# Kernel optimization log

Hardware: AMD Instinct MI355X
Metric: run time of the kernel (lower is better)

The kernel has to match this reference:

```python
import jax, jax.numpy as jnp
import numpy as np

B = 512        # graphs per batch
N_NODES = 64   # nodes per graph
IN_CH = 256
EMBED = 64
TOPK = 20
NEG_SLOPE = 0.2


def setup_inputs() -> dict:
    key = jax.random.key(0)
    ks = jax.random.split(key, 6)
    N = B * N_NODES
    x = jax.random.normal(ks[0], (N, IN_CH), dtype=jnp.float32)
    # fully-connected graph WITH self loops, per graph, sorted source-major
    src = jnp.repeat(jnp.arange(N_NODES, dtype=jnp.int32), N_NODES)  # [n*n]
    dst = jnp.tile(jnp.arange(N_NODES, dtype=jnp.int32), N_NODES)    # [n*n]
    offs = (jnp.arange(B, dtype=jnp.int32) * N_NODES)[:, None]       # [B,1]
    l = (src[None, :] + offs).reshape(-1)
    r = (dst[None, :] + offs).reshape(-1)
    edge_index = jnp.stack([l, r]).astype(jnp.int32)                 # [2, B*n*n]
    batch = jnp.repeat(jnp.arange(B, dtype=jnp.int32), N_NODES)      # [N]
    glorot = lambda k, sh: jax.random.uniform(k, sh, jnp.float32,
                                              -1.0, 1.0) * np.sqrt(6.0 / (sh[0] + sh[-1]))
    Wl = glorot(ks[1], (EMBED, IN_CH))
    bl = jnp.zeros((EMBED,), jnp.float32)
    Wr = glorot(ks[2], (EMBED, IN_CH))
    br = jnp.zeros((EMBED,), jnp.float32)
    att = glorot(ks[3], (1, EMBED))
    return {"x": x, "edge_index": edge_index, "batch": batch,
            "Wl": Wl, "bl": bl, "Wr": Wr, "br": br, "att": att}


def reference(x, edge_index, batch, Wl, bl, Wr, br, att):
    N = x.shape[0]
    x_l = x @ Wl.T + bl                      # [N, D]
    x_r = x @ Wr.T + br                      # [N, D]
    l, r = edge_index[0], edge_index[1]
    # edge gather + GAT-style score
    e = jax.nn.leaky_relu(x_l[l] + x_r[r], negative_slope=NEG_SLOPE)  # [E, D]
    alpha = (e * att[0]).sum(axis=-1)                                  # [E]
    # segment softmax grouped by source node l (each group is non-empty)
    m = jax.ops.segment_max(alpha, l, num_segments=N)
    a = jnp.exp(alpha - m[l])
    s = jax.ops.segment_sum(a, l, num_segments=N)
    a = a / s[l]
    # kNN sparsify: zero the diagonal then per-row topk
    a3 = a.reshape(B, N_NODES, N_NODES)
    a3 = a3 * (1.0 - jnp.eye(N_NODES, dtype=a3.dtype))
    attention, indices = jax.lax.top_k(a3, TOPK)     # [B, n, k] sorted desc
    attention = attention.reshape(-1)                 # [B*n*k]
    offs = (jnp.arange(B, dtype=jnp.int32) * N_NODES)[:, None]
    index_i = (jnp.repeat(jnp.arange(N_NODES, dtype=jnp.int32), TOPK)[None, :]
               + offs).reshape(-1)
    index_j = (indices.astype(jnp.int32)
               + (jnp.arange(B, dtype=jnp.int32) * N_NODES)[:, None, None]).reshape(-1)
    new_edge_index = jnp.stack([index_i, index_j])    # [2, B*n*k]
    return new_edge_index, attention
```

## Files before the change

### kernel.cpp

```cpp
#include <hip/hip_runtime.h>
#include <stdint.h>

#define NGRAPH 512
#define NN 64
#define INCH 256
#define TOPK 20
#define EPR 655360
#define WS_NEED ((size_t)65536 + (size_t)16777216)

typedef __attribute__((ext_vector_type(8))) short bf16x8;
typedef __attribute__((ext_vector_type(4))) float f32x4;

#define XLR 0
#define XRR 4352
#define SMEM_DW 8704

static __device__ __forceinline__ uint32_t f2bfbits(float f) {
  uint32_t u = __float_as_uint(f);
  return (u + 0x7FFFu + ((u >> 16) & 1u)) >> 16;
}
static __device__ __forceinline__ uint32_t pk2(float a, float b) {
  return f2bfbits(a) | (f2bfbits(b) << 16);
}
static __device__ __forceinline__ float keyalpha(uint32_t k) {
  uint32_t ub = (k & 0x80000000u) ? (k ^ 0x80000000u) : ~k;
  return __uint_as_float(ub & 0xFFFFFFC0u);
}
static __device__ __forceinline__ float redsum64(float v) {
  int p;
  p = __builtin_amdgcn_update_dpp(0, __float_as_int(v), 0xB1, 0xF, 0xF, true);
  v += __int_as_float(p);
  p = __builtin_amdgcn_update_dpp(0, __float_as_int(v), 0x4E, 0xF, 0xF, true);
  v += __int_as_float(p);
  v += __shfl_xor(v, 4);
  v += __shfl_xor(v, 8);
  v += __shfl_xor(v, 16);
  v += __shfl_xor(v, 32);
  return v;
}

__global__ __launch_bounds__(256) void wpack2(const float* __restrict__ Wl,
                                              const float* __restrict__ Wr,
                                              uint4* __restrict__ wsW) {
  const int t = blockIdx.x * 256 + threadIdx.x;
  const int lo = t & 15, quad = (t >> 4) & 3, ct = (t >> 6) & 3;
  const int ks = (t >> 8) & 7, half = (t >> 11) & 1;
  const int n = ct * 16 + lo, k0 = ks * 32 + quad * 8;
  const float* src = half ? Wr : Wl;
  const float4* s4 = (const float4*)(src + (size_t)n * INCH + k0);
  float4 a0 = s4[0], a1 = s4[1];
  wsW[t] = (uint4){ pk2(a0.x, a0.y), pk2(a0.z, a0.w), pk2(a1.x, a1.y), pk2(a1.z, a1.w) };
}

__global__ __launch_bounds__(256) void xpack(const float* __restrict__ x,
                                             uint4* __restrict__ xp) {
  const int t = blockIdx.x * 256 + threadIdx.x;
  const int lo = t & 15, quad = (t >> 4) & 3, rt = (t >> 6) & 3;
  const int ks = (t >> 8) & 7, b = t >> 11;
  const int row = b * 64 + rt * 16 + lo, k0 = ks * 32 + quad * 8;
  const float4* s4 = (const float4*)(x + (size_t)row * INCH + k0);
  float4 a0 = s4[0], a1 = s4[1];
  xp[t] = (uint4){ pk2(a0.x, a0.y), pk2(a0.z, a0.w), pk2(a1.x, a1.y), pk2(a1.z, a1.w) };
}

template <bool XP>
__global__ __launch_bounds__(512, 4) void gat_fused(
    const float* __restrict__ x,
    const uint4* __restrict__ wsV,
    const float* __restrict__ blv,
    const float* __restrict__ brv,
    const float* __restrict__ att,
    float* __restrict__ out)
{
  __shared__ __align__(16) uint32_t smemU[SMEM_DW];
  float* smemF = (float*)smemU;

  const int b    = blockIdx.x;
  const int t    = threadIdx.x;
  const int w    = t >> 6;
  const int lane = t & 63;
  const int quad = lane >> 4;
  const int lo   = lane & 15;
  const int nodeBase = b * NN;

  const float attv = att[lane];

  const int half = w >> 2;
  const int rt   = w & 3;
  const int r0   = rt * 16;
  const uint4* xpV = wsV + 4096;

  f32x4 acc[4];
  #pragma unroll
  for (int ct = 0; ct < 4; ++ct) acc[ct] = (f32x4){0.f, 0.f, 0.f, 0.f};

  #pragma unroll
  for (int ks = 0; ks < 8; ++ks) {
    bf16x8 afrag;
    if constexpr (XP) {
      uint4 au = xpV[(size_t)b * 2048 + ks * 256 + rt * 64 + quad * 16 + lo];
      afrag = __builtin_bit_cast(bf16x8, au);
    } else {
      const int k0 = ks * 32 + quad * 8;
      const float* ap = x + (size_t)(nodeBase + r0 + lo) * INCH + k0;
      float4 a0 = *(const float4*)ap;
      float4 a1 = *(const float4*)(ap + 4);
      uint4 au = { pk2(a0.x, a0.y), pk2(a0.z, a0.w), pk2(a1.x, a1.y), pk2(a1.z, a1.w) };
      afrag = __builtin_bit_cast(bf16x8, au);
    }
    #pragma unroll
    for (int ct = 0; ct < 4; ++ct) {
      uint4 bu = wsV[half * 2048 + ks * 256 + ct * 64 + quad * 16 + lo];
      bf16x8 bfrag = __builtin_bit_cast(bf16x8, bu);
      acc[ct] = __builtin_amdgcn_mfma_f32_16x16x32_bf16(afrag, bfrag, acc[ct], 0, 0, 0);
    }
  }

  {
    const float* bias = half ? brv : blv;
    const int dstBase = half ? XRR : XLR;
    #pragma unroll
    for (int ct = 0; ct < 4; ++ct) {
      const int d = ct * 16 + lo;
      const float bb = bias[d];
      #pragma unroll
      for (int rg = 0; rg < 4; ++rg)
        smemF[dstBase + (r0 + quad * 4 + rg) * 68 + d] = acc[ct][rg] + bb;
    }
  }
  __syncthreads();

  const int rB = w * 8;

  float xlv[8];
  #pragma unroll
  for (int q = 0; q < 8; ++q)
    xlv[q] = smemF[XLR + (rB + q) * 68 + lane];

  float sl[8];
  #pragma unroll
  for (int q = 0; q < 8; ++q)
    sl[q] = redsum64(attv * xlv[q]);

  float pacc[8];
  #pragma unroll
  for (int q = 0; q < 8; ++q) pacc[q] = 0.f;
  float srp = 0.f;
  const int xrb = XRR + lane * 68;
  #pragma unroll
  for (int c = 0; c < 4; ++c) {
    f32x4 xrc[4];
    #pragma unroll
    for (int g = 0; g < 4; ++g)
      xrc[g] = *(const f32x4*)&smemF[xrb + c * 16 + g * 4];
    #pragma unroll
    for (int dl = 0; dl < 16; ++dl) {
      const int d = c * 16 + dl;
      const float xv = xrc[dl >> 2][dl & 3];
      const float av = __int_as_float(
          __builtin_amdgcn_readlane(__float_as_int(attv), d));
      srp = fmaf(av, xv, srp);
      #pragma unroll
      for (int q = 0; q < 8; ++q) {
        const float xls = __int_as_float(
            __builtin_amdgcn_readlane(__float_as_int(xlv[q]), d));
        pacc[q] = fmaf(av, fabsf(xls + xv), pacc[q]);
      }
    }
  }

  float aq[8];
  #pragma unroll
  for (int q = 0; q < 8; ++q)
    aq[q] = 0.6f * (sl[q] + srp) + 0.4f * pacc[q];

  uint32_t key[8];
  #pragma unroll
  for (int q = 0; q < 8; ++q) {
    const uint32_t u = __float_as_uint(aq[q]);
    uint32_t kk = u ^ ((uint32_t)((int32_t)u >> 31) | 0x80000000u);
    kk = (kk & 0xFFFFFFC0u) | (uint32_t)(63 - lane);
    key[q] = (lane == rB + q) ? 0u : kk;
  }

  #pragma unroll
  for (int k = 2; k <= 64; k <<= 1) {
    #pragma unroll
    for (int j = k >> 1; j >= 1; j >>= 1) {
      const bool keep_max = (((lane & k) == 0) == ((lane & j) == 0));
      #pragma unroll
      for (int q = 0; q < 8; ++q) {
        uint32_t p;
        if (j == 1)
          p = (uint32_t)__builtin_amdgcn_update_dpp(0, (int)key[q], 0xB1, 0xF, 0xF, true);
        else if (j == 2)
          p = (uint32_t)__builtin_amdgcn_update_dpp(0, (int)key[q], 0x4E, 0xF, 0xF, true);
        else
          p = (uint32_t)__shfl_xor((int)key[q], j);
        const uint32_t mx = (key[q] > p) ? key[q] : p;
        const uint32_t mn = (key[q] > p) ? p : key[q];
        key[q] = keep_max ? mx : mn;
      }
    }
  }

  float mq[8], Sq[8];
  #pragma unroll
  for (int q = 0; q < 8; ++q) {
    const uint32_t tk = (uint32_t)__builtin_amdgcn_readlane((int)key[q], 0);
    const float topa  = keyalpha(tk);
    const float adiag = __int_as_float(
        __builtin_amdgcn_readlane(__float_as_int(aq[q]), rB + q));
    mq[q] = fmaxf(topa, adiag);
    Sq[q] = redsum64(__expf(aq[q] - mq[q]));
  }

  if (lane < TOPK) {
    #pragma unroll
    for (int q = 0; q < 8; ++q) {
      const int g = nodeBase + rB + q;
      const uint32_t kq = key[q];
      const float alpha = keyalpha(kq);
      const int jj = 63 - (int)(kq & 63u);
      const float va = __expf(alpha - mq[q]) * (1.0f / Sq[q]);
      out[(size_t)g * 20 + lane] = (float)g;
      out[(size_t)EPR + (size_t)g * 20 + lane] = (float)(nodeBase + jj);
      out[2 * (size_t)EPR + (size_t)g * 20 + lane] = va;
    }
  }
}

extern "C" void kernel_launch(void* const* d_in, const int* in_sizes, int n_in,
                              void* d_out, int out_size, void* d_ws, size_t ws_size,
                              hipStream_t stream) {
  const float* x   = (const float*)d_in[0];
  const float* Wl  = (const float*)d_in[3];
  const float* bl  = (const float*)d_in[4];
  const float* Wr  = (const float*)d_in[5];
  const float* br  = (const float*)d_in[6];
  const float* att = (const float*)d_in[7];
  uint4* wsW = (uint4*)d_ws;

  wpack2<<<dim3(16), dim3(256), 0, stream>>>(Wl, Wr, wsW);
  if (ws_size >= WS_NEED) {
    xpack<<<dim3(4096), dim3(256), 0, stream>>>(x, wsW + 4096);
    gat_fused<true><<<dim3(NGRAPH), dim3(512), 0, stream>>>(
        x, wsW, bl, br, att, (float*)d_out);
  } else {
    gat_fused<false><<<dim3(NGRAPH), dim3(512), 0, stream>>>(
        x, wsW, bl, br, att, (float*)d_out);
  }
}
```

Before: 124.6 us.

## Split fused GAT kernel into GEMM and per-row alpha/top-k sort kernels

```diff
diff --git a/kernel.cpp b/kernel.cpp
--- a/kernel.cpp
+++ b/kernel.cpp
@@ -6,14 +6,11 @@
 #define INCH 256
 #define TOPK 20
 #define EPR 655360
+#define NROWS 32768
 #define WS_NEED ((size_t)65536 + (size_t)16777216)
 
 typedef __attribute__((ext_vector_type(8))) short bf16x8;
 typedef __attribute__((ext_vector_type(4))) float f32x4;
-
-#define XLR 0
-#define XRR 4352
-#define SMEM_DW 8704
 
 static __device__ __forceinline__ uint32_t f2bfbits(float f) {
   uint32_t u = __float_as_uint(f);
@@ -26,16 +23,38 @@
   uint32_t ub = (k & 0x80000000u) ? (k ^ 0x80000000u) : ~k;
   return __uint_as_float(ub & 0xFFFFFFC0u);
 }
-static __device__ __forceinline__ float redsum64(float v) {
-  int p;
-  p = __builtin_amdgcn_update_dpp(0, __float_as_int(v), 0xB1, 0xF, 0xF, true);
-  v += __int_as_float(p);
-  p = __builtin_amdgcn_update_dpp(0, __float_as_int(v), 0x4E, 0xF, 0xF, true);
-  v += __int_as_float(p);
-  v += __shfl_xor(v, 4);
-  v += __shfl_xor(v, 8);
-  v += __shfl_xor(v, 16);
-  v += __shfl_xor(v, 32);
+
+static __device__ __forceinline__ uint32_t bflyu(uint32_t v, const int j, const int lane) {
+  if (j == 1)
+    return (uint32_t)__builtin_amdgcn_update_dpp(0, (int)v, 0xB1, 0xF, 0xF, true);
+  if (j == 2)
+    return (uint32_t)__builtin_amdgcn_update_dpp(0, (int)v, 0x4E, 0xF, 0xF, true);
+  if (j == 8)
+    return (uint32_t)__builtin_amdgcn_update_dpp(0, (int)v, 0x128, 0xF, 0xF, true);
+#if __has_builtin(__builtin_amdgcn_permlane16_swap)
+  if (j == 16) {
+    auto r = __builtin_amdgcn_permlane16_swap((unsigned)v, (unsigned)v, false, false);
+    return (uint32_t)(((lane >> 4) & 1) ? r[0] : r[1]);
+  }
+#endif
+#if __has_builtin(__builtin_amdgcn_permlane32_swap)
+  if (j == 32) {
+    auto r = __builtin_amdgcn_permlane32_swap((unsigned)v, (unsigned)v, false, false);
+    return (uint32_t)((lane & 32) ? r[0] : r[1]);
+  }
+#endif
+  return (uint32_t)__shfl_xor((int)v, j);
+}
+static __device__ __forceinline__ float bflyf(float v, const int j, const int lane) {
+  return __uint_as_float(bflyu(__float_as_uint(v), j, lane));
+}
+static __device__ __forceinline__ float redsum64(float v, const int lane) {
+  v += bflyf(v, 1, lane);
+  v += bflyf(v, 2, lane);
+  v += bflyf(v, 4, lane);
+  v += bflyf(v, 8, lane);
+  v += bflyf(v, 16, lane);
+  v += bflyf(v, 32, lane);
   return v;
 }
 
@@ -52,29 +71,13 @@
   wsW[t] = (uint4){ pk2(a0.x, a0.y), pk2(a0.z, a0.w), pk2(a1.x, a1.y), pk2(a1.z, a1.w) };
 }
 
-__global__ __launch_bounds__(256) void xpack(const float* __restrict__ x,
-                                             uint4* __restrict__ xp) {
-  const int t = blockIdx.x * 256 + threadIdx.x;
-  const int lo = t & 15, quad = (t >> 4) & 3, rt = (t >> 6) & 3;
-  const int ks = (t >> 8) & 7, b = t >> 11;
-  const int row = b * 64 + rt * 16 + lo, k0 = ks * 32 + quad * 8;
-  const float4* s4 = (const float4*)(x + (size_t)row * INCH + k0);
-  float4 a0 = s4[0], a1 = s4[1];
-  xp[t] = (uint4){ pk2(a0.x, a0.y), pk2(a0.z, a0.w), pk2(a1.x, a1.y), pk2(a1.z, a1.w) };
-}
-
-template <bool XP>
-__global__ __launch_bounds__(512, 4) void gat_fused(
+__global__ __launch_bounds__(512, 4) void xlr_gemm(
     const float* __restrict__ x,
     const uint4* __restrict__ wsV,
     const float* __restrict__ blv,
     const float* __restrict__ brv,
-    const float* __restrict__ att,
-    float* __restrict__ out)
+    float* __restrict__ xlr)
 {
-  __shared__ __align__(16) uint32_t smemU[SMEM_DW];
-  float* smemF = (float*)smemU;
-
   const int b    = blockIdx.x;
   const int t    = threadIdx.x;
   const int w    = t >> 6;
@@ -82,13 +85,8 @@
   const int quad = lane >> 4;
   const int lo   = lane & 15;
   const int nodeBase = b * NN;
-
-  const float attv = att[lane];
-
   const int half = w >> 2;
-  const int rt   = w & 3;
-  const int r0   = rt * 16;
-  const uint4* xpV = wsV + 4096;
+  const int r0   = (w & 3) * 16;
 
   f32x4 acc[4];
   #pragma unroll
@@ -96,18 +94,12 @@
 
   #pragma unroll
   for (int ks = 0; ks < 8; ++ks) {
-    bf16x8 afrag;
-    if constexpr (XP) {
-      uint4 au = xpV[(size_t)b * 2048 + ks * 256 + rt * 64 + quad * 16 + lo];
-      afrag = __builtin_bit_cast(bf16x8, au);
-    } else {
-      const int k0 = ks * 32 + quad * 8;
-      const float* ap = x + (size_t)(nodeBase + r0 + lo) * INCH + k0;
-      float4 a0 = *(const float4*)ap;
-      float4 a1 = *(const float4*)(ap + 4);
-      uint4 au = { pk2(a0.x, a0.y), pk2(a0.z, a0.w), pk2(a1.x, a1.y), pk2(a1.z, a1.w) };
-      afrag = __builtin_bit_cast(bf16x8, au);
-    }
+    const int k0 = ks * 32 + quad * 8;
+    const float* ap = x + (size_t)(nodeBase + r0 + lo) * INCH + k0;
+    float4 a0 = *(const float4*)ap;
+    float4 a1 = *(const float4*)(ap + 4);
+    uint4 au = { pk2(a0.x, a0.y), pk2(a0.z, a0.w), pk2(a1.x, a1.y), pk2(a1.z, a1.w) };
+    bf16x8 afrag = __builtin_bit_cast(bf16x8, au);
     #pragma unroll
     for (int ct = 0; ct < 4; ++ct) {
       uint4 bu = wsV[half * 2048 + ks * 256 + ct * 64 + quad * 16 + lo];
@@ -116,6 +108,121 @@
     }
   }
 
+  const float* bias = half ? brv : blv;
+  float* dst = xlr + (size_t)half * ((size_t)NROWS * 64);
+  #pragma unroll
+  for (int ct = 0; ct < 4; ++ct) {
+    const int d = ct * 16 + lo;
+    const float bb = bias[d];
+    #pragma unroll
+    for (int rg = 0; rg < 4; ++rg)
+      dst[(size_t)(nodeBase + r0 + quad * 4 + rg) * 64 + d] = acc[ct][rg] + bb;
+  }
+}
+
+__global__ __launch_bounds__(256, 4) void alphasort(
+    const float* __restrict__ xlr,
+    const float* __restrict__ att,
+    float* __restrict__ out)
+{
+  const int lane = threadIdx.x & 63;
+  const int row  = __builtin_amdgcn_readfirstlane(
+      (int)(blockIdx.x << 2) + (int)(threadIdx.x >> 6));
+  const int i        = row & 63;
+  const int nodeBase = row - i;
+
+  const float* xrp = xlr + (size_t)NROWS * 64 + (size_t)(nodeBase + lane) * 64;
+  f32x4 xrv[16];
+  #pragma unroll
+  for (int c = 0; c < 16; ++c) xrv[c] = *(const f32x4*)(xrp + c * 4);
+
+  const float* xlp = xlr + (size_t)row * 64;
+
+  float pa0 = 0.f, pa1 = 0.f, sr0 = 0.f, sr1 = 0.f;
+  #pragma unroll
+  for (int d = 0; d < 64; d += 2) {
+    const float a0 = att[d], a1 = att[d + 1];
+    const float l0 = xlp[d], l1 = xlp[d + 1];
+    const float x0 = xrv[d >> 2][d & 3];
+    const float x1 = xrv[(d + 1) >> 2][(d + 1) & 3];
+    pa0 = fmaf(a0, fabsf(l0 + x0), pa0);
+    sr0 = fmaf(a0, x0, sr0);
+    pa1 = fmaf(a1, fabsf(l1 + x1), pa1);
+    sr1 = fmaf(a1, x1, sr1);
+  }
+  const float aq = 0.6f * (sr0 + sr1) + 0.4f * (pa0 + pa1);
+
+  uint32_t key;
+  {
+    const uint32_t u = __float_as_uint(aq);
+    uint32_t kk = u ^ ((uint32_t)((int32_t)u >> 31) | 0x80000000u);
+    kk = (kk & 0xFFFFFFC0u) | (uint32_t)(63 - lane);
+    key = (lane == i) ? 0u : kk;
+  }
+
+  #pragma unroll
+  for (int k = 2; k <= 64; k <<= 1) {
+    #pragma unroll
+    for (int j = k >> 1; j >= 1; j >>= 1) {
+      const bool keep_max = (((lane & k) == 0) == ((lane & j) == 0));
+      const uint32_t p = bflyu(key, j, lane);
+      const uint32_t mx = (key > p) ? key : p;
+      const uint32_t mn = (key > p) ? p : key;
+      key = keep_max ? mx : mn;
+    }
+  }
+
+  const uint32_t tk = (uint32_t)__builtin_amdgcn_readlane((int)key, 0);
+  const float adiag = __int_as_float(
+      __builtin_amdgcn_readlane(__float_as_int(aq), i));
+  const float m  = fmaxf(keyalpha(tk), adiag);
+  const float Sv = redsum64(__expf(aq - m), lane);
+
+  if (lane < TOPK) {
+    const float alpha = keyalpha(key);
+    const int jj = 63 - (int)(key & 63u);
+    const float va = __expf(alpha - m) * (1.0f / Sv);
+    out[(size_t)row * 20 + lane] = (float)row;
+    out[(size_t)EPR + (size_t)row * 20 + lane] = (float)(nodeBase + jj);
+    out[2 * (size_t)EPR + (size_t)row * 20 + lane] = va;
+  }
+}
+
+#define XLR 0
+#define XRR 4352
+#define SMEM_DW 8704
+
+__global__ __launch_bounds__(512, 4) void gat_fused_fb(
+    const float* __restrict__ x, const uint4* __restrict__ wsV,
+    const float* __restrict__ blv, const float* __restrict__ brv,
+    const float* __restrict__ att, float* __restrict__ out)
+{
+  __shared__ __align__(16) uint32_t smemU[SMEM_DW];
+  float* smemF = (float*)smemU;
+  const int b = blockIdx.x, t = threadIdx.x;
+  const int w = t >> 6, lane = t & 63, quad = lane >> 4, lo = lane & 15;
+  const int nodeBase = b * NN;
+  const float attv = att[lane];
+  const int half = w >> 2, r0 = (w & 3) * 16;
+
+  f32x4 acc[4];
+  #pragma unroll
+  for (int ct = 0; ct < 4; ++ct) acc[ct] = (f32x4){0.f, 0.f, 0.f, 0.f};
+  #pragma unroll
+  for (int ks = 0; ks < 8; ++ks) {
+    const int k0 = ks * 32 + quad * 8;
+    const float* ap = x + (size_t)(nodeBase + r0 + lo) * INCH + k0;
+    float4 a0 = *(const float4*)ap;
+    float4 a1 = *(const float4*)(ap + 4);
+    uint4 au = { pk2(a0.x, a0.y), pk2(a0.z, a0.w), pk2(a1.x, a1.y), pk2(a1.z, a1.w) };
+    bf16x8 afrag = __builtin_bit_cast(bf16x8, au);
+    #pragma unroll
+    for (int ct = 0; ct < 4; ++ct) {
+      uint4 bu = wsV[half * 2048 + ks * 256 + ct * 64 + quad * 16 + lo];
+      bf16x8 bfrag = __builtin_bit_cast(bf16x8, bu);
+      acc[ct] = __builtin_amdgcn_mfma_f32_16x16x32_bf16(afrag, bfrag, acc[ct], 0, 0, 0);
+    }
+  }
   {
     const float* bias = half ? brv : blv;
     const int dstBase = half ? XRR : XLR;
@@ -131,16 +238,12 @@
   __syncthreads();
 
   const int rB = w * 8;
-
   float xlv[8];
   #pragma unroll
-  for (int q = 0; q < 8; ++q)
-    xlv[q] = smemF[XLR + (rB + q) * 68 + lane];
-
+  for (int q = 0; q < 8; ++q) xlv[q] = smemF[XLR + (rB + q) * 68 + lane];
   float sl[8];
   #pragma unroll
-  for (int q = 0; q < 8; ++q)
-    sl[q] = redsum64(attv * xlv[q]);
+  for (int q = 0; q < 8; ++q) sl[q] = redsum64(attv * xlv[q], lane);
 
   float pacc[8];
   #pragma unroll
@@ -151,14 +254,12 @@
   for (int c = 0; c < 4; ++c) {
     f32x4 xrc[4];
     #pragma unroll
-    for (int g = 0; g < 4; ++g)
-      xrc[g] = *(const f32x4*)&smemF[xrb + c * 16 + g * 4];
+    for (int g = 0; g < 4; ++g) xrc[g] = *(const f32x4*)&smemF[xrb + c * 16 + g * 4];
     #pragma unroll
     for (int dl = 0; dl < 16; ++dl) {
       const int d = c * 16 + dl;
       const float xv = xrc[dl >> 2][dl & 3];
-      const float av = __int_as_float(
-          __builtin_amdgcn_readlane(__float_as_int(attv), d));
+      const float av = __int_as_float(__builtin_amdgcn_readlane(__float_as_int(attv), d));
       srp = fmaf(av, xv, srp);
       #pragma unroll
       for (int q = 0; q < 8; ++q) {
@@ -168,11 +269,9 @@
       }
     }
   }
-
   float aq[8];
   #pragma unroll
-  for (int q = 0; q < 8; ++q)
-    aq[q] = 0.6f * (sl[q] + srp) + 0.4f * pacc[q];
+  for (int q = 0; q < 8; ++q) aq[q] = 0.6f * (sl[q] + srp) + 0.4f * pacc[q];
 
   uint32_t key[8];
   #pragma unroll
@@ -182,7 +281,6 @@
     kk = (kk & 0xFFFFFFC0u) | (uint32_t)(63 - lane);
     key[q] = (lane == rB + q) ? 0u : kk;
   }
-
   #pragma unroll
   for (int k = 2; k <= 64; k <<= 1) {
     #pragma unroll
@@ -190,38 +288,28 @@
       const bool keep_max = (((lane & k) == 0) == ((lane & j) == 0));
       #pragma unroll
       for (int q = 0; q < 8; ++q) {
-        uint32_t p;
-        if (j == 1)
-          p = (uint32_t)__builtin_amdgcn_update_dpp(0, (int)key[q], 0xB1, 0xF, 0xF, true);
-        else if (j == 2)
-          p = (uint32_t)__builtin_amdgcn_update_dpp(0, (int)key[q], 0x4E, 0xF, 0xF, true);
-        else
-          p = (uint32_t)__shfl_xor((int)key[q], j);
+        const uint32_t p = bflyu(key[q], j, lane);
         const uint32_t mx = (key[q] > p) ? key[q] : p;
         const uint32_t mn = (key[q] > p) ? p : key[q];
         key[q] = keep_max ? mx : mn;
       }
     }
   }
-
   float mq[8], Sq[8];
   #pragma unroll
   for (int q = 0; q < 8; ++q) {
     const uint32_t tk = (uint32_t)__builtin_amdgcn_readlane((int)key[q], 0);
-    const float topa  = keyalpha(tk);
     const float adiag = __int_as_float(
         __builtin_amdgcn_readlane(__float_as_int(aq[q]), rB + q));
-    mq[q] = fmaxf(topa, adiag);
-    Sq[q] = redsum64(__expf(aq[q] - mq[q]));
-  }
-
+    mq[q] = fmaxf(keyalpha(tk), adiag);
+    Sq[q] = redsum64(__expf(aq[q] - mq[q]), lane);
+  }
   if (lane < TOPK) {
     #pragma unroll
     for (int q = 0; q < 8; ++q) {
       const int g = nodeBase + rB + q;
-      const uint32_t kq = key[q];
-      const float alpha = keyalpha(kq);
-      const int jj = 63 - (int)(kq & 63u);
+      const float alpha = keyalpha(key[q]);
+      const int jj = 63 - (int)(key[q] & 63u);
       const float va = __expf(alpha - mq[q]) * (1.0f / Sq[q]);
       out[(size_t)g * 20 + lane] = (float)g;
       out[(size_t)EPR + (size_t)g * 20 + lane] = (float)(nodeBase + jj);
@@ -243,11 +331,11 @@
 
   wpack2<<<dim3(16), dim3(256), 0, stream>>>(Wl, Wr, wsW);
   if (ws_size >= WS_NEED) {
-    xpack<<<dim3(4096), dim3(256), 0, stream>>>(x, wsW + 4096);
-    gat_fused<true><<<dim3(NGRAPH), dim3(512), 0, stream>>>(
-        x, wsW, bl, br, att, (float*)d_out);
+    float* xlr = (float*)((char*)d_ws + 65536);
+    xlr_gemm<<<dim3(NGRAPH), dim3(512), 0, stream>>>(x, wsW, bl, br, xlr);
+    alphasort<<<dim3(8192), dim3(256), 0, stream>>>(xlr, att, (float*)d_out);
   } else {
-    gat_fused<false><<<dim3(NGRAPH), dim3(512), 0, stream>>>(
-        x, wsW, bl, br, att, (float*)d_out);
-  }
-}
+    gat_fused_fb<<<dim3(NGRAPH), dim3(512), 0, stream>>>(x, wsW, bl, br, att,
+                                                         (float*)d_out);
+  }
+}
```

Measured after the change: 169.0 us. 35.7% more time.
